# Optimization experiments

Hardware: AMD Instinct MI355X
Metric: run time of the kernel (lower is better)

Reference implementation:

```python
import jax, jax.numpy as jnp
import numpy as np

B, N, F = 256, 64, 64
S = 2 * N + 2  # seq_len = N*2 + 2 = 130
EPS = 1e-6
SCALE = float(np.sqrt(S))


def _norm(x, alpha, beta):
    # custom Norm: mean/std over last axis, affine params shaped (F, S)
    m = jnp.mean(x, axis=-1, keepdims=True)
    s = jnp.std(x, axis=-1, keepdims=True)
    return alpha * (x - m) / (s + EPS) + beta


def setup_inputs() -> dict:
    key = jax.random.key(0)
    ks = jax.random.split(key, 12)
    d = {
        "sp": jax.random.normal(ks[0], (B, F), jnp.float32),
        "h1": jax.random.normal(ks[1], (B, N, F), jnp.float32),
        "h2": jax.random.normal(ks[2], (B, N, F), jnp.float32),
        # Dense(seq_len) kernels act on last axis of length S
        "Wq": jax.random.normal(ks[3], (S, S), jnp.float32) * 0.05,
        "bq": jnp.zeros((S,), jnp.float32),
        "Wk": jax.random.normal(ks[4], (S, S), jnp.float32) * 0.05,
        "bk": jnp.zeros((S,), jnp.float32),
        "Wv": jax.random.normal(ks[5], (S, S), jnp.float32) * 0.05,
        "bv": jnp.zeros((S,), jnp.float32),
        "alpha1": jnp.ones((F, S), jnp.float32),
        "beta1": jnp.zeros((F, S), jnp.float32),
        "alpha2": jnp.ones((F, S), jnp.float32),
        "beta2": jnp.zeros((F, S), jnp.float32),
        "Wlin": jax.random.normal(ks[6], (F * S, 1), jnp.float32) * 0.02,
        "blin": jnp.zeros((1,), jnp.float32),
    }
    return d


def reference(sp, h1, h2, Wq, bq, Wk, bk, Wv, bv,
              alpha1, beta1, alpha2, beta2, Wlin, blin):
    # obs: (B, 2N+1, F) -> transpose -> (B, F, 2N+1)
    obs = jnp.concatenate((h1, h2, sp[:, None, :]), axis=1).transpose(0, 2, 1)
    h2t = h2.transpose(0, 2, 1)  # (B, F, N): each action is a (B, F) column

    def fwd_action(action):  # action: (B, F)
        x = jnp.concatenate((obs, action[:, :, None]), axis=-1)  # (B, F, S)
        xn = _norm(x, alpha1, beta1)
        q = xn @ Wq + bq  # (B, F, S)
        k = xn @ Wk + bk
        v = xn @ Wv + bv
        # attention over the FEATURE axis: scores (B, F, F)
        sim = jnp.einsum('bis,bjs->bij', q, k) / SCALE
        p = jax.nn.softmax(sim, axis=-1)
        ao = jnp.einsum('bij,bjs->bis', p, v)  # (B, F, S)
        # deterministic dropout => residual is ao + ao
        y = _norm(ao + ao, alpha2, beta2)
        return y.reshape(B, -1) @ Wlin + blin  # (B, 1)

    q_values = jax.vmap(fwd_action, in_axes=-1, out_axes=1)(h2t)  # (B, N, 1)
    return q_values.reshape(B, N)
```

## Files before the change

kernel.cpp:

```cpp
#include <hip/hip_runtime.h>
#include <math.h>


typedef __attribute__((ext_vector_type(4))) float f32x4;
typedef __attribute__((ext_vector_type(8))) short bf16x8;

#define EPSF 1e-6f
#define INVS 0.0877058019307029f

__device__ __forceinline__ unsigned short f2bf(float f) {
  unsigned int u = __builtin_bit_cast(unsigned int, f);
  u += 0x7FFFu + ((u >> 16) & 1u);
  return (unsigned short)(u >> 16);
}
__device__ __forceinline__ float b2f(unsigned short s) {
  unsigned int u = ((unsigned int)s) << 16;
  return __builtin_bit_cast(float, u);
}
__device__ __forceinline__ unsigned int pk2(float a, float b) {
  unsigned int r;
  asm("v_cvt_pk_bf16_f32 %0, %1, %2" : "=v"(r) : "v"(a), "v"(b));
  return r;
}

__global__ __launch_bounds__(256) void k0(
    const float* __restrict__ alpha1, const float* __restrict__ beta1,
    const float* __restrict__ alpha2, const float* __restrict__ beta2,
    const float* __restrict__ Wq, const float* __restrict__ bq,
    const float* __restrict__ Wk, const float* __restrict__ bk,
    const float* __restrict__ Wv, const float* __restrict__ bv,
    const float* __restrict__ Wlin, const float* __restrict__ blin,
    unsigned short* __restrict__ ABqk, unsigned short* __restrict__ ABv,
    unsigned short* __restrict__ AWt, float* __restrict__ Paw, float* __restrict__ Ccw)
{
  __shared__ float sbuf[64 * 132];
  __shared__ float Wbuf[130 * 144];
  int blk = blockIdx.x, tid = threadIdx.x;
  if (blk < 6) {
    int m = blk >> 1, isB = blk & 1;
    const float* src  = isB ? beta1 : alpha1;
    const float* W    = (m == 0) ? Wq : (m == 1) ? Wk : Wv;
    const float* bias = (m == 0) ? bq : (m == 1) ? bk : bv;
    for (int e = tid; e < 8320; e += 256) { int f = e / 130, s = e - f * 130; sbuf[f * 132 + s] = src[e]; }
    for (int e = tid; e < 16900; e += 256) { int s = e / 130, t = e - s * 130; Wbuf[s * 144 + t] = W[e]; }
    __syncthreads();
    int ty = tid >> 4, tx = tid & 15;
    float acc[4][9] = {};
    for (int s = 0; s < 130; ++s) {
      float g0 = sbuf[(ty * 4 + 0) * 132 + s];
      float g1 = sbuf[(ty * 4 + 1) * 132 + s];
      float g2 = sbuf[(ty * 4 + 2) * 132 + s];
      float g3 = sbuf[(ty * 4 + 3) * 132 + s];
#pragma unroll
      for (int c = 0; c < 9; ++c) {
        float wv = Wbuf[s * 144 + tx + 16 * c];
        acc[0][c] += g0 * wv; acc[1][c] += g1 * wv;
        acc[2][c] += g2 * wv; acc[3][c] += g3 * wv;
      }
    }
#pragma unroll
    for (int i = 0; i < 4; ++i)
      for (int c = 0; c < 9; ++c) {
        int t = tx + 16 * c;
        if (t < 136) {
          float val = (t < 130) ? (acc[i][c] + (isB ? bias[t] : 0.f)) : 0.f;
          unsigned short v16 = f2bf(val);
          int f = ty * 4 + i;
          if (m == 2) ABv[t * 128 + isB * 64 + f] = v16;
          else        ABqk[(m * 64 + f) * 272 + (t >> 3) * 16 + isB * 8 + (t & 7)] = v16;
        }
      }
  } else if (blk == 6) {
    if (tid < 64) {
      int f = tid;
      float pa = 0.f, cc = 0.f;
      for (int s = 0; s < 130; ++s) {
        float wl = Wlin[f * 130 + s];
        float aw = alpha2[f * 130 + s] * wl;
        AWt[s * 72 + f] = f2bf(aw);
        pa += aw;
        cc += beta2[f * 130 + s] * wl;
      }
      for (int s = 130; s < 144; ++s) AWt[s * 72 + f] = 0;
      Paw[f] = pa;
#pragma unroll
      for (int msk = 1; msk <= 32; msk <<= 1) cc += __shfl_xor(cc, msk, 64);
      if (f == 0) Ccw[0] = cc + blin[0];
    }
  }
}

__global__ __launch_bounds__(256) void k1(
    const float* __restrict__ h1, const float* __restrict__ h2,
    const float* __restrict__ sp, const float* __restrict__ alpha1,
    const float* __restrict__ Wq, const float* __restrict__ Wk, const float* __restrict__ Wv,
    unsigned short* __restrict__ UqkB, unsigned short* __restrict__ UvB,
    float* __restrict__ S1g, float* __restrict__ S2g)
{
  __shared__ float gbuf[64 * 132];
  __shared__ float Wbuf[130 * 144];
  __shared__ float ps[2][256];
  int b = blockIdx.x, tid = threadIdx.x;
  float s1 = 0.f, s2 = 0.f;
  for (int idx = tid; idx < 8256; idx += 256) {
    int s = idx >> 6, f = idx & 63;
    float x = (s < 64)  ? h1[((size_t)(b * 64 + s)) * 64 + f]
            : (s < 128) ? h2[((size_t)(b * 64 + (s - 64))) * 64 + f]
                        : sp[b * 64 + f];
    gbuf[f * 132 + s] = alpha1[f * 130 + s] * x;
    s1 += x; s2 += x * x;
  }
  ps[0][tid] = s1; ps[1][tid] = s2;
  __syncthreads();
  if (tid < 64) {
    S1g[b * 64 + tid] = ps[0][tid] + ps[0][tid + 64] + ps[0][tid + 128] + ps[0][tid + 192];
    S2g[b * 64 + tid] = ps[1][tid] + ps[1][tid + 64] + ps[1][tid + 128] + ps[1][tid + 192];
  }
  int ty = tid >> 4, tx = tid & 15;
  for (int m = 0; m < 3; ++m) {
    const float* W = (m == 0) ? Wq : (m == 1) ? Wk : Wv;
    __syncthreads();
    for (int e = tid; e < 16900; e += 256) { int s = e / 130, t = e - s * 130; Wbuf[s * 144 + t] = W[e]; }
    __syncthreads();
    float acc[4][9] = {};
    for (int s = 0; s < 129; ++s) {
      float g0 = gbuf[(ty * 4 + 0) * 132 + s];
      float g1 = gbuf[(ty * 4 + 1) * 132 + s];
      float g2 = gbuf[(ty * 4 + 2) * 132 + s];
      float g3 = gbuf[(ty * 4 + 3) * 132 + s];
#pragma unroll
      for (int c = 0; c < 9; ++c) {
        float wv = Wbuf[s * 144 + tx + 16 * c];
        acc[0][c] += g0 * wv; acc[1][c] += g1 * wv;
        acc[2][c] += g2 * wv; acc[3][c] += g3 * wv;
      }
    }
#pragma unroll
    for (int i = 0; i < 4; ++i)
      for (int c = 0; c < 9; ++c) {
        int t = tx + 16 * c;
        if (t < 136) {
          unsigned short v16 = f2bf((t < 130) ? acc[i][c] : 0.f);
          int f = ty * 4 + i;
          if (m == 2) UvB[((size_t)b * 136 + t) * 64 + f] = v16;
          else        UqkB[(((size_t)b * 2 + m) * 64 + f) * 136 + t] = v16;
        }
      }
  }
}

__global__ __launch_bounds__(512, 2) void k2(
    const float* __restrict__ h2, const float* __restrict__ alpha1,
    const unsigned short* __restrict__ UqkB, const unsigned short* __restrict__ UvB,
    const unsigned short* __restrict__ ABqk, const unsigned short* __restrict__ ABv,
    const unsigned short* __restrict__ AWt,
    const float* __restrict__ S1g, const float* __restrict__ S2g,
    const float* __restrict__ Paw, const float* __restrict__ Ccw,
    const float* __restrict__ Wq, const float* __restrict__ Wk, const float* __restrict__ Wv,
    float* __restrict__ out)
{
  __shared__ __align__(16) unsigned short qb[64 * 168];
  __shared__ __align__(16) unsigned short kb[64 * 168];
  __shared__ __align__(16) unsigned short vT[144 * 72];
  __shared__ __align__(16) unsigned short pb[64 * 72];
  __shared__ __align__(16) unsigned short uqk_l[2 * 64 * 136];
  __shared__ __align__(16) unsigned short uv_l[136 * 64];
  __shared__ __align__(16) float w129l[3][136];
  __shared__ float S1l[64], S2l[64], ael[64];
  __shared__ float mrow[64], irow[64], crow[64];
  __shared__ float redbuf[4];

  int b = blockIdx.x, tid = threadIdx.x;
  int w = tid >> 6, l = tid & 63, l15 = l & 15, l4 = l >> 4;

  if (tid < 136) {
    w129l[0][tid] = (tid < 130) ? Wq[129 * 130 + tid] : 0.f;
    w129l[1][tid] = (tid < 130) ? Wk[129 * 130 + tid] : 0.f;
    w129l[2][tid] = (tid < 130) ? Wv[129 * 130 + tid] : 0.f;
  }
  if (tid >= 256 && tid < 320) {
    int ff = tid - 256;
    float s1v = S1g[b * 64 + ff];
    float s2v = S2g[b * 64 + ff];
    float aev = alpha1[ff * 130 + 129];
    S1l[ff] = s1v; S2l[ff] = s2v; ael[ff] = aev;
    float a  = h2[((size_t)(b * 64 + 0)) * 64 + ff];
    float m  = (s1v + a) * (1.f / 130.f);
    float e2 = (s2v + a * a) * (1.f / 130.f);
    float sd = sqrtf(fmaxf(e2 - m * m, 0.f));
    mrow[ff] = m;
    irow[ff] = 1.f / (sd + EPSF);
    crow[ff] = aev * a;
  }
  {
    const uint4* src = (const uint4*)(UqkB + ((size_t)b * 2) * 64 * 136);
    uint4* dst = (uint4*)uqk_l;
    for (int i = tid; i < 2176; i += 512) dst[i] = src[i];
  }
  {
    const uint4* src = (const uint4*)(UvB + (size_t)b * 136 * 64);
    uint4* dst = (uint4*)uv_l;
    for (int i = tid; i < 1088; i += 512) dst[i] = src[i];
  }
  for (int i = tid; i < 64 * 24; i += 512) {
    int ff = i / 24, t = 136 + (i - ff * 24);
    qb[ff * 168 + t] = 0; kb[ff * 168 + t] = 0;
  }
  for (int i = tid; i < 14 * 72; i += 512) vT[130 * 72 + i] = 0;

  float awr[9][4], pawr[4];
  if (w < 4) {
#pragma unroll
    for (int sf = 0; sf < 9; ++sf)
#pragma unroll
      for (int r = 0; r < 4; ++r)
        awr[sf][r] = b2f(AWt[(sf * 16 + l15) * 72 + w * 16 + l4 * 4 + r]);
#pragma unroll
    for (int r = 0; r < 4; ++r) pawr[r] = Paw[w * 16 + l4 * 4 + r];
  }
  float ccv = Ccw[0];

  int isK = tid >> 8, t5 = tid & 255;
  const unsigned short* abg = ABqk + isK * 64 * 272;
  unsigned short* dstqk = isK ? kb : qb;

  __syncthreads();

  auto genqk = [&](int o) {
    int fo = o / 17, g = o - fo * 17;
    float m = mrow[fo], inv = irow[fo], c = crow[fo];
    bf16x8 uu = *(const bf16x8*)(uqk_l + (isK * 64 + fo) * 136 + g * 8);
    bf16x8 aa = *(const bf16x8*)(abg + fo * 272 + g * 16);
    bf16x8 bb = *(const bf16x8*)(abg + fo * 272 + g * 16 + 8);
    f32x4 w0 = *(const f32x4*)&w129l[isK][g * 8];
    f32x4 w1 = *(const f32x4*)&w129l[isK][g * 8 + 4];
    float v[8];
#pragma unroll
    for (int e = 0; e < 4; ++e)
      v[e] = (b2f(uu[e]) + c * w0[e] - m * b2f(aa[e])) * inv + b2f(bb[e]);
#pragma unroll
    for (int e = 0; e < 4; ++e)
      v[4 + e] = (b2f(uu[4 + e]) + c * w1[e] - m * b2f(aa[4 + e])) * inv + b2f(bb[4 + e]);
    uint4 ov;
    ov.x = pk2(v[0], v[1]); ov.y = pk2(v[2], v[3]);
    ov.z = pk2(v[4], v[5]); ov.w = pk2(v[6], v[7]);
    *(uint4*)(dstqk + fo * 168 + g * 8) = ov;
  };
  auto genv = [&](int o) {
    int t = o >> 3, vf = o & 7;
    float wv = w129l[2][t];
    bf16x8 uu = *(const bf16x8*)(uv_l + t * 64 + vf * 8);
    bf16x8 aa = *(const bf16x8*)(ABv + t * 128 + vf * 8);
    bf16x8 bb = *(const bf16x8*)(ABv + t * 128 + 64 + vf * 8);
    f32x4 m0 = *(const f32x4*)&mrow[vf * 8], m1 = *(const f32x4*)&mrow[vf * 8 + 4];
    f32x4 i0 = *(const f32x4*)&irow[vf * 8], i1 = *(const f32x4*)&irow[vf * 8 + 4];
    f32x4 c0 = *(const f32x4*)&crow[vf * 8], c1 = *(const f32x4*)&crow[vf * 8 + 4];
    float v[8];
#pragma unroll
    for (int e = 0; e < 4; ++e)
      v[e] = (b2f(uu[e]) + c0[e] * wv - m0[e] * b2f(aa[e])) * i0[e] + b2f(bb[e]);
#pragma unroll
    for (int e = 0; e < 4; ++e)
      v[4 + e] = (b2f(uu[4 + e]) + c1[e] * wv - m1[e] * b2f(aa[4 + e])) * i1[e] + b2f(bb[4 + e]);
    uint4 ov;
    ov.x = pk2(v[0], v[1]); ov.y = pk2(v[2], v[3]);
    ov.z = pk2(v[4], v[5]); ov.w = pk2(v[6], v[7]);
    *(uint4*)&vT[t * 72 + vf * 8] = ov;
  };

  for (int n = 0; n < 64; ++n) {
    if (n > 0 && tid == 0)
      out[b * 64 + n - 1] = redbuf[0] + redbuf[1] + redbuf[2] + redbuf[3] + ccv;
#pragma unroll
    for (int kg = 0; kg < 4; ++kg) genqk(t5 + (kg << 8));
    if (t5 < 64) genqk(1024 + t5);
    genv(tid); genv(tid + 512);
    if (tid < 16) genv(1024 + tid);
    __syncthreads();

    if (w < 4) {
      f32x4 sacc[4] = {};
      {
        const unsigned short* qrow = &qb[(w * 16 + l15) * 168 + l4 * 8];
#pragma unroll
        for (int kk = 0; kk < 5; ++kk) {
          bf16x8 avv = *(const bf16x8*)&qrow[kk * 32];
#pragma unroll
          for (int cf = 0; cf < 4; ++cf) {
            bf16x8 bvv = *(const bf16x8*)&kb[(cf * 16 + l15) * 168 + l4 * 8 + kk * 32];
            sacc[cf] = __builtin_amdgcn_mfma_f32_16x16x32_bf16(avv, bvv, sacc[cf], 0, 0, 0);
          }
        }
      }
      float prob[4][4];
#pragma unroll
      for (int r = 0; r < 4; ++r) {
        float ssum = 0.f;
#pragma unroll
        for (int cf = 0; cf < 4; ++cf) {
          float e = __expf(sacc[cf][r] * INVS);
          prob[cf][r] = e;
          ssum += e;
        }
#pragma unroll
        for (int msk = 1; msk <= 8; msk <<= 1) ssum += __shfl_xor(ssum, msk, 64);
        float is = 1.f / ssum;
#pragma unroll
        for (int cf = 0; cf < 4; ++cf) prob[cf][r] *= is;
      }
#pragma unroll
      for (int cf = 0; cf < 4; ++cf) {
        unsigned int p01 = pk2(prob[cf][0], prob[cf][1]);
        unsigned int p23 = pk2(prob[cf][2], prob[cf][3]);
        int base = (w * 16 + l4 * 4) * 72 + cf * 16 + l15;
        pb[base]       = (unsigned short)p01;
        pb[base + 72]  = (unsigned short)(p01 >> 16);
        pb[base + 144] = (unsigned short)p23;
        pb[base + 216] = (unsigned short)(p23 >> 16);
      }

      f32x4 ao[9] = {};
      {
        const unsigned short* prow = &pb[(w * 16 + l15) * 72 + l4 * 8];
#pragma unroll
        for (int kk = 0; kk < 2; ++kk) {
          bf16x8 avv = *(const bf16x8*)&prow[kk * 32];
#pragma unroll
          for (int sf = 0; sf < 9; ++sf) {
            bf16x8 bvv = *(const bf16x8*)&vT[(sf * 16 + l15) * 72 + l4 * 8 + kk * 32];
            ao[sf] = __builtin_amdgcn_mfma_f32_16x16x32_bf16(avv, bvv, ao[sf], 0, 0, 0);
          }
        }
      }
      float csum = 0.f;
#pragma unroll
      for (int r = 0; r < 4; ++r) {
        float s1 = 0.f, s2 = 0.f, sdt = 0.f;
#pragma unroll
        for (int sf = 0; sf < 9; ++sf) {
          float v = ao[sf][r];
          s1 += v; s2 += v * v; sdt += v * awr[sf][r];
        }
#pragma unroll
        for (int msk = 1; msk <= 8; msk <<= 1) {
          s1 += __shfl_xor(s1, msk, 64);
          s2 += __shfl_xor(s2, msk, 64);
          sdt += __shfl_xor(sdt, msk, 64);
        }
        float mz  = 2.f * s1 * (1.f / 130.f);
        float ez2 = 4.f * s2 * (1.f / 130.f);
        float sg  = sqrtf(fmaxf(ez2 - mz * mz, 0.f));
        float i2  = 1.f / (sg + EPSF);
        csum += (2.f * sdt - mz * pawr[r]) * i2;
      }
      csum += __shfl_xor(csum, 16, 64);
      csum += __shfl_xor(csum, 32, 64);
      if (l == 0) redbuf[w] = csum;
    } else if (w == 4 && n < 63) {
      int ff = l;
      float a  = h2[((size_t)(b * 64 + n + 1)) * 64 + ff];
      float m  = (S1l[ff] + a) * (1.f / 130.f);
      float e2 = (S2l[ff] + a * a) * (1.f / 130.f);
      float sd = sqrtf(fmaxf(e2 - m * m, 0.f));
      mrow[ff] = m;
      irow[ff] = 1.f / (sd + EPSF);
      crow[ff] = ael[ff] * a;
    }
    __syncthreads();
  }
  if (tid == 0)
    out[b * 64 + 63] = redbuf[0] + redbuf[1] + redbuf[2] + redbuf[3] + ccv;
}

extern "C" void kernel_launch(void* const* d_in, const int* in_sizes, int n_in,
                              void* d_out, int out_size, void* d_ws, size_t ws_size,
                              hipStream_t stream) {
  const float* sp     = (const float*)d_in[0];
  const float* h1     = (const float*)d_in[1];
  const float* h2     = (const float*)d_in[2];
  const float* Wq     = (const float*)d_in[3];
  const float* bq     = (const float*)d_in[4];
  const float* Wk     = (const float*)d_in[5];
  const float* bk     = (const float*)d_in[6];
  const float* Wv     = (const float*)d_in[7];
  const float* bv     = (const float*)d_in[8];
  const float* alpha1 = (const float*)d_in[9];
  const float* beta1  = (const float*)d_in[10];
  const float* beta2  = (const float*)d_in[12];
  const float* alpha2 = (const float*)d_in[11];
  const float* Wlin   = (const float*)d_in[13];
  const float* blin   = (const float*)d_in[14];
  float* out = (float*)d_out;

  unsigned short* UqkB = (unsigned short*)d_ws;
  unsigned short* UvB  = UqkB + 4456448;
  unsigned short* ABqk = UvB + 2228224;
  unsigned short* ABv  = ABqk + 34816;
  unsigned short* AWt  = ABv + 17408;
  float* S1g = (float*)(AWt + 10368);
  float* S2g = S1g + 16384;
  float* Paw = S2g + 16384;
  float* Ccw = Paw + 64;

  k0<<<dim3(7), dim3(256), 0, stream>>>(alpha1, beta1, alpha2, beta2,
                                        Wq, bq, Wk, bk, Wv, bv, Wlin, blin,
                                        ABqk, ABv, AWt, Paw, Ccw);
  k1<<<dim3(256), dim3(256), 0, stream>>>(h1, h2, sp, alpha1, Wq, Wk, Wv,
                                          UqkB, UvB, S1g, S2g);
  k2<<<dim3(256), dim3(512), 0, stream>>>(h2, alpha1, UqkB, UvB, ABqk, ABv, AWt,
                                          S1g, S2g, Paw, Ccw,
                                          Wq, Wk, Wv, out);
}
```

Measured before the change: 373.4 us.

## Switch intermediate storage and MFMA from bf16 to fp16 with packed-half elementwise math

Converts every stored intermediate (U, AB tables, AW weights, per-row stats, q/k/v/p tiles) from bf16 to fp16 and uses the f16 MFMA instructions. The per-action q/k/v generation is rewritten to do its affine normalisation in packed half-precision vector arithmetic rather than unpacking to fp32 and repacking, which cuts ALU and conversion work in the inner loop. In exchange, the normalisation math now runs in fp16, and the fp16 range and precision differ from bf16, which risks accuracy loss or overflow.

```diff
diff --git a/kernel.cpp b/kernel.cpp
--- a/kernel.cpp
+++ b/kernel.cpp
@@ -3,23 +3,21 @@
 
 
 typedef __attribute__((ext_vector_type(4))) float f32x4;
-typedef __attribute__((ext_vector_type(8))) short bf16x8;
+typedef __attribute__((ext_vector_type(8))) _Float16 h8;
 
 #define EPSF 1e-6f
 #define INVS 0.0877058019307029f
 
-__device__ __forceinline__ unsigned short f2bf(float f) {
-  unsigned int u = __builtin_bit_cast(unsigned int, f);
-  u += 0x7FFFu + ((u >> 16) & 1u);
-  return (unsigned short)(u >> 16);
-}
-__device__ __forceinline__ float b2f(unsigned short s) {
-  unsigned int u = ((unsigned int)s) << 16;
-  return __builtin_bit_cast(float, u);
-}
-__device__ __forceinline__ unsigned int pk2(float a, float b) {
+__device__ __forceinline__ unsigned short f2h(float f) {
+  _Float16 h = (_Float16)f;
+  return __builtin_bit_cast(unsigned short, h);
+}
+__device__ __forceinline__ float h2f(unsigned short s) {
+  return (float)__builtin_bit_cast(_Float16, s);
+}
+__device__ __forceinline__ unsigned int pkh(float a, float b) {
   unsigned int r;
-  asm("v_cvt_pk_bf16_f32 %0, %1, %2" : "=v"(r) : "v"(a), "v"(b));
+  asm("v_cvt_pkrtz_f16_f32 %0, %1, %2" : "=v"(r) : "v"(a), "v"(b));
   return r;
 }
 
@@ -64,7 +62,7 @@
         int t = tx + 16 * c;
         if (t < 136) {
           float val = (t < 130) ? (acc[i][c] + (isB ? bias[t] : 0.f)) : 0.f;
-          unsigned short v16 = f2bf(val);
+          unsigned short v16 = f2h(val);
           int f = ty * 4 + i;
           if (m == 2) ABv[t * 128 + isB * 64 + f] = v16;
           else        ABqk[(m * 64 + f) * 272 + (t >> 3) * 16 + isB * 8 + (t & 7)] = v16;
@@ -77,7 +75,7 @@
       for (int s = 0; s < 130; ++s) {
         float wl = Wlin[f * 130 + s];
         float aw = alpha2[f * 130 + s] * wl;
-        AWt[s * 72 + f] = f2bf(aw);
+        AWt[s * 72 + f] = f2h(aw);
         pa += aw;
         cc += beta2[f * 130 + s] * wl;
       }
@@ -140,7 +138,7 @@
       for (int c = 0; c < 9; ++c) {
         int t = tx + 16 * c;
         if (t < 136) {
-          unsigned short v16 = f2bf((t < 130) ? acc[i][c] : 0.f);
+          unsigned short v16 = f2h((t < 130) ? acc[i][c] : 0.f);
           int f = ty * 4 + i;
           if (m == 2) UvB[((size_t)b * 136 + t) * 64 + f] = v16;
           else        UqkB[(((size_t)b * 2 + m) * 64 + f) * 136 + t] = v16;
@@ -165,18 +163,18 @@
   __shared__ __align__(16) unsigned short pb[64 * 72];
   __shared__ __align__(16) unsigned short uqk_l[2 * 64 * 136];
   __shared__ __align__(16) unsigned short uv_l[136 * 64];
-  __shared__ __align__(16) float w129l[3][136];
+  __shared__ __align__(16) unsigned short w129h[3][136];
   __shared__ float S1l[64], S2l[64], ael[64];
-  __shared__ float mrow[64], irow[64], crow[64];
+  __shared__ __align__(16) unsigned short mrow[64], irow[64], crow[64];
   __shared__ float redbuf[4];
 
   int b = blockIdx.x, tid = threadIdx.x;
   int w = tid >> 6, l = tid & 63, l15 = l & 15, l4 = l >> 4;
 
   if (tid < 136) {
-    w129l[0][tid] = (tid < 130) ? Wq[129 * 130 + tid] : 0.f;
-    w129l[1][tid] = (tid < 130) ? Wk[129 * 130 + tid] : 0.f;
-    w129l[2][tid] = (tid < 130) ? Wv[129 * 130 + tid] : 0.f;
+    w129h[0][tid] = (tid < 130) ? f2h(Wq[129 * 130 + tid]) : (unsigned short)0;
+    w129h[1][tid] = (tid < 130) ? f2h(Wk[129 * 130 + tid]) : (unsigned short)0;
+    w129h[2][tid] = (tid < 130) ? f2h(Wv[129 * 130 + tid]) : (unsigned short)0;
   }
   if (tid >= 256 && tid < 320) {
     int ff = tid - 256;
@@ -188,9 +186,9 @@
     float m  = (s1v + a) * (1.f / 130.f);
     float e2 = (s2v + a * a) * (1.f / 130.f);
     float sd = sqrtf(fmaxf(e2 - m * m, 0.f));
-    mrow[ff] = m;
-    irow[ff] = 1.f / (sd + EPSF);
-    crow[ff] = aev * a;
+    mrow[ff] = f2h(m);
+    irow[ff] = f2h(1.f / (sd + EPSF));
+    crow[ff] = f2h(aev * a);
   }
   {
     const uint4* src = (const uint4*)(UqkB + ((size_t)b * 2) * 64 * 136);
@@ -213,10 +211,10 @@
 #pragma unroll
     for (int sf = 0; sf < 9; ++sf)
 #pragma unroll
-      for (int r = 0; r < 4; ++r)
-        awr[sf][r] = b2f(AWt[(sf * 16 + l15) * 72 + w * 16 + l4 * 4 + r]);
-#pragma unroll
-    for (int r = 0; r < 4; ++r) pawr[r] = Paw[w * 16 + l4 * 4 + r];
+      for (int rr = 0; rr < 4; ++rr)
+        awr[sf][rr] = h2f(AWt[(sf * 16 + l15) * 72 + w * 16 + l4 * 4 + rr]);
+#pragma unroll
+    for (int rr = 0; rr < 4; ++rr) pawr[rr] = Paw[w * 16 + l4 * 4 + rr];
   }
   float ccv = Ccw[0];
 
@@ -228,44 +226,27 @@
 
   auto genqk = [&](int o) {
     int fo = o / 17, g = o - fo * 17;
-    float m = mrow[fo], inv = irow[fo], c = crow[fo];
-    bf16x8 uu = *(const bf16x8*)(uqk_l + (isK * 64 + fo) * 136 + g * 8);
-    bf16x8 aa = *(const bf16x8*)(abg + fo * 272 + g * 16);
-    bf16x8 bb = *(const bf16x8*)(abg + fo * 272 + g * 16 + 8);
-    f32x4 w0 = *(const f32x4*)&w129l[isK][g * 8];
-    f32x4 w1 = *(const f32x4*)&w129l[isK][g * 8 + 4];
-    float v[8];
-#pragma unroll
-    for (int e = 0; e < 4; ++e)
-      v[e] = (b2f(uu[e]) + c * w0[e] - m * b2f(aa[e])) * inv + b2f(bb[e]);
-#pragma unroll
-    for (int e = 0; e < 4; ++e)
-      v[4 + e] = (b2f(uu[4 + e]) + c * w1[e] - m * b2f(aa[4 + e])) * inv + b2f(bb[4 + e]);
-    uint4 ov;
-    ov.x = pk2(v[0], v[1]); ov.y = pk2(v[2], v[3]);
-    ov.z = pk2(v[4], v[5]); ov.w = pk2(v[6], v[7]);
-    *(uint4*)(dstqk + fo * 168 + g * 8) = ov;
+    _Float16 m = __builtin_bit_cast(_Float16, mrow[fo]);
+    _Float16 inv = __builtin_bit_cast(_Float16, irow[fo]);
+    _Float16 c = __builtin_bit_cast(_Float16, crow[fo]);
+    h8 uu = *(const h8*)(uqk_l + (isK * 64 + fo) * 136 + g * 8);
+    h8 aa = *(const h8*)(abg + fo * 272 + g * 16);
+    h8 bb = *(const h8*)(abg + fo * 272 + g * 16 + 8);
+    h8 ww = *(const h8*)(&w129h[isK][g * 8]);
+    h8 res = (uu + c * ww - m * aa) * inv + bb;
+    *(h8*)(dstqk + fo * 168 + g * 8) = res;
   };
   auto genv = [&](int o) {
     int t = o >> 3, vf = o & 7;
-    float wv = w129l[2][t];
-    bf16x8 uu = *(const bf16x8*)(uv_l + t * 64 + vf * 8);
-    bf16x8 aa = *(const bf16x8*)(ABv + t * 128 + vf * 8);
-    bf16x8 bb = *(const bf16x8*)(ABv + t * 128 + 64 + vf * 8);
-    f32x4 m0 = *(const f32x4*)&mrow[vf * 8], m1 = *(const f32x4*)&mrow[vf * 8 + 4];
-    f32x4 i0 = *(const f32x4*)&irow[vf * 8], i1 = *(const f32x4*)&irow[vf * 8 + 4];
-    f32x4 c0 = *(const f32x4*)&crow[vf * 8], c1 = *(const f32x4*)&crow[vf * 8 + 4];
-    float v[8];
-#pragma unroll
-    for (int e = 0; e < 4; ++e)
-      v[e] = (b2f(uu[e]) + c0[e] * wv - m0[e] * b2f(aa[e])) * i0[e] + b2f(bb[e]);
-#pragma unroll
-    for (int e = 0; e < 4; ++e)
-      v[4 + e] = (b2f(uu[4 + e]) + c1[e] * wv - m1[e] * b2f(aa[4 + e])) * i1[e] + b2f(bb[4 + e]);
-    uint4 ov;
-    ov.x = pk2(v[0], v[1]); ov.y = pk2(v[2], v[3]);
-    ov.z = pk2(v[4], v[5]); ov.w = pk2(v[6], v[7]);
-    *(uint4*)&vT[t * 72 + vf * 8] = ov;
+    _Float16 wv = __builtin_bit_cast(_Float16, w129h[2][t]);
+    h8 uu = *(const h8*)(uv_l + t * 64 + vf * 8);
+    h8 aa = *(const h8*)(ABv + t * 128 + vf * 8);
+    h8 bb = *(const h8*)(ABv + t * 128 + 64 + vf * 8);
+    h8 mv = *(const h8*)(&mrow[vf * 8]);
+    h8 iv = *(const h8*)(&irow[vf * 8]);
+    h8 cv = *(const h8*)(&crow[vf * 8]);
+    h8 res = (uu + cv * wv - mv * aa) * iv + bb;
+    *(h8*)(&vT[t * 72 + vf * 8]) = res;
   };
 
   for (int n = 0; n < 64; ++n) {
@@ -284,34 +265,34 @@
         const unsigned short* qrow = &qb[(w * 16 + l15) * 168 + l4 * 8];
 #pragma unroll
         for (int kk = 0; kk < 5; ++kk) {
-          bf16x8 avv = *(const bf16x8*)&qrow[kk * 32];
+          h8 avv = *(const h8*)&qrow[kk * 32];
 #pragma unroll
           for (int cf = 0; cf < 4; ++cf) {
-            bf16x8 bvv = *(const bf16x8*)&kb[(cf * 16 + l15) * 168 + l4 * 8 + kk * 32];
-            sacc[cf] = __builtin_amdgcn_mfma_f32_16x16x32_bf16(avv, bvv, sacc[cf], 0, 0, 0);
+            h8 bvv = *(const h8*)&kb[(cf * 16 + l15) * 168 + l4 * 8 + kk * 32];
+            sacc[cf] = __builtin_amdgcn_mfma_f32_16x16x32_f16(avv, bvv, sacc[cf], 0, 0, 0);
           }
         }
       }
       float prob[4][4];
 #pragma unroll
-      for (int r = 0; r < 4; ++r) {
+      for (int rr = 0; rr < 4; ++rr) {
         float ssum = 0.f;
 #pragma unroll
         for (int cf = 0; cf < 4; ++cf) {
-          float e = __expf(sacc[cf][r] * INVS);
-          prob[cf][r] = e;
+          float e = __expf(sacc[cf][rr] * INVS);
+          prob[cf][rr] = e;
           ssum += e;
         }
 #pragma unroll
         for (int msk = 1; msk <= 8; msk <<= 1) ssum += __shfl_xor(ssum, msk, 64);
         float is = 1.f / ssum;
 #pragma unroll
-        for (int cf = 0; cf < 4; ++cf) prob[cf][r] *= is;
+        for (int cf = 0; cf < 4; ++cf) prob[cf][rr] *= is;
       }
 #pragma unroll
       for (int cf = 0; cf < 4; ++cf) {
-        unsigned int p01 = pk2(prob[cf][0], prob[cf][1]);
-        unsigned int p23 = pk2(prob[cf][2], prob[cf][3]);
+        unsigned int p01 = pkh(prob[cf][0], prob[cf][1]);
+        unsigned int p23 = pkh(prob[cf][2], prob[cf][3]);
         int base = (w * 16 + l4 * 4) * 72 + cf * 16 + l15;
         pb[base]       = (unsigned short)p01;
         pb[base + 72]  = (unsigned short)(p01 >> 16);
@@ -324,22 +305,22 @@
         const unsigned short* prow = &pb[(w * 16 + l15) * 72 + l4 * 8];
 #pragma unroll
         for (int kk = 0; kk < 2; ++kk) {
-          bf16x8 avv = *(const bf16x8*)&prow[kk * 32];
+          h8 avv = *(const h8*)&prow[kk * 32];
 #pragma unroll
           for (int sf = 0; sf < 9; ++sf) {
-            bf16x8 bvv = *(const bf16x8*)&vT[(sf * 16 + l15) * 72 + l4 * 8 + kk * 32];
-            ao[sf] = __builtin_amdgcn_mfma_f32_16x16x32_bf16(avv, bvv, ao[sf], 0, 0, 0);
+            h8 bvv = *(const h8*)&vT[(sf * 16 + l15) * 72 + l4 * 8 + kk * 32];
+            ao[sf] = __builtin_amdgcn_mfma_f32_16x16x32_f16(avv, bvv, ao[sf], 0, 0, 0);
           }
         }
       }
       float csum = 0.f;
 #pragma unroll
-      for (int r = 0; r < 4; ++r) {
+      for (int rr = 0; rr < 4; ++rr) {
         float s1 = 0.f, s2 = 0.f, sdt = 0.f;
 #pragma unroll
         for (int sf = 0; sf < 9; ++sf) {
-          float v = ao[sf][r];
-          s1 += v; s2 += v * v; sdt += v * awr[sf][r];
+          float v = ao[sf][rr];
+          s1 += v; s2 += v * v; sdt += v * awr[sf][rr];
         }
 #pragma unroll
         for (int msk = 1; msk <= 8; msk <<= 1) {
@@ -351,7 +332,7 @@
         float ez2 = 4.f * s2 * (1.f / 130.f);
         float sg  = sqrtf(fmaxf(ez2 - mz * mz, 0.f));
         float i2  = 1.f / (sg + EPSF);
-        csum += (2.f * sdt - mz * pawr[r]) * i2;
+        csum += (2.f * sdt - mz * pawr[rr]) * i2;
       }
       csum += __shfl_xor(csum, 16, 64);
       csum += __shfl_xor(csum, 32, 64);
@@ -362,9 +343,9 @@
       float m  = (S1l[ff] + a) * (1.f / 130.f);
       float e2 = (S2l[ff] + a * a) * (1.f / 130.f);
       float sd = sqrtf(fmaxf(e2 - m * m, 0.f));
-      mrow[ff] = m;
-      irow[ff] = 1.f / (sd + EPSF);
-      crow[ff] = ael[ff] * a;
+      mrow[ff] = f2h(m);
+      irow[ff] = f2h(1.f / (sd + EPSF));
+      crow[ff] = f2h(ael[ff] * a);
     }
     __syncthreads();
   }
@@ -386,8 +367,8 @@
   const float* bv     = (const float*)d_in[8];
   const float* alpha1 = (const float*)d_in[9];
   const float* beta1  = (const float*)d_in[10];
+  const float* alpha2 = (const float*)d_in[11];
   const float* beta2  = (const float*)d_in[12];
-  const float* alpha2 = (const float*)d_in[11];
   const float* Wlin   = (const float*)d_in[13];
   const float* blin   = (const float*)d_in[14];
   float* out = (float*)d_out;
```

Result: faster. 327.3 us (-12.4%).
